# Kernel optimization log

Hardware: AMD Instinct MI355X
Metric: run time of the kernel (lower is better)

Reference implementation:

```python
import jax, jax.numpy as jnp
import numpy as np

B, N, E = 2, 10000, 160000
NODE_DIM, EDGE_DIM, HIDDEN = 128, 64, 256


def setup_inputs() -> dict:
    key = jax.random.key(0)
    ks = jax.random.split(key, 12)
    def lin(k, fan_in, fan_out):
        return jax.random.normal(k, (fan_in, fan_out), dtype=jnp.float32) / np.sqrt(fan_in)
    msg_in = 2 * NODE_DIM + EDGE_DIM   # 320
    upd_in = NODE_DIM + HIDDEN         # 384
    return {
        "node_features": jax.random.normal(ks[0], (B, N, NODE_DIM), dtype=jnp.float32),
        "edge_indices": jax.random.randint(ks[1], (B, E, 2), 0, N, dtype=jnp.int32),
        "edge_features": jax.random.normal(ks[2], (B, E, EDGE_DIM), dtype=jnp.float32),
        "W1m": lin(ks[3], msg_in, HIDDEN),  "b1m": jnp.zeros((HIDDEN,), jnp.float32),
        "W2m": lin(ks[4], HIDDEN, HIDDEN),  "b2m": jnp.zeros((HIDDEN,), jnp.float32),
        "W1u": lin(ks[5], upd_in, HIDDEN),  "b1u": jnp.zeros((HIDDEN,), jnp.float32),
        "W2u": lin(ks[6], HIDDEN, NODE_DIM), "b2u": jnp.zeros((NODE_DIM,), jnp.float32),
    }


def reference(node_features, edge_indices, edge_features,
              W1m, b1m, W2m, b2m, W1u, b1u, W2u, b2u):
    # node_features: [B, N, D]; edge_indices: [B, E, 2]; edge_features: [B, E, F]
    b, n, d = node_features.shape
    e = edge_indices.shape[1]
    src_idx = edge_indices[..., 0]  # [B, E]
    dst_idx = edge_indices[..., 1]  # [B, E]
    # batched gather of endpoint features
    src = jnp.take_along_axis(node_features, src_idx[..., None], axis=1)  # [B, E, D]
    dst = jnp.take_along_axis(node_features, dst_idx[..., None], axis=1)  # [B, E, D]
    msg_in = jnp.concatenate([src, dst, edge_features], axis=-1)          # [B, E, 2D+F]
    h = jax.nn.gelu(jnp.einsum("bei,ih->beh", msg_in, W1m) + b1m)
    messages = jnp.einsum("beh,ho->beo", h, W2m) + b2m                    # [B, E, H]
    # scatter-add into destination node buckets (flatten batch for segment_sum)
    flat_dst = (dst_idx + (jnp.arange(b, dtype=dst_idx.dtype)[:, None] * n)).reshape(-1)
    aggregated = jax.ops.segment_sum(
        messages.reshape(b * e, -1), flat_dst, num_segments=b * n
    ).reshape(b, n, -1)                                                   # [B, N, H]
    upd_in = jnp.concatenate([node_features, aggregated], axis=-1)        # [B, N, D+H]
    u = jax.nn.gelu(jnp.einsum("bni,ih->bnh", upd_in, W1u) + b1u)
    return jnp.einsum("bnh,ho->bno", u, W2u) + b2u                        # [B, N, D]
```

## Files before the change

### kernel.cpp

```cpp
#include <hip/hip_runtime.h>
#include <hip/hip_bf16.h>
#include <math.h>

#define BATCH   2
#define N_NODES 10000
#define E_EDGES 160000
#define BN      (BATCH * N_NODES)
#define BE      (BATCH * E_EDGES)
#define ND      128
#define ED      64
#define HID     256
#define K1      320
#define K2      256
#define K1U     384
#define NOUT    128
#define TMN     32
#define TME     64
#define LDH     264

typedef __attribute__((ext_vector_type(8))) short bf16x8;
typedef __attribute__((ext_vector_type(4))) float f32x4;

__device__ unsigned short g_Pb[(size_t)BN * 512];
__device__ unsigned short g_nodef_bf[(size_t)BN * ND];
__device__ unsigned short g_w1c[HID * K1U];
__device__ unsigned short g_w2ut[K2 * NOUT];
__device__ float          g_bc[HID];
__device__ int            g_hist[BN];

__device__ __forceinline__ float gelu_tanh(float x) {
    float u = 0.7978845608028654f * (x + 0.044715f * x * x * x);
    float e = __expf(2.0f * u);
    float t = 1.0f - 2.0f * __builtin_amdgcn_rcpf(e + 1.0f);
    return 0.5f * x * (1.0f + t);
}

__device__ __forceinline__ unsigned short f2bf(float f) {
    __hip_bfloat16 h = __float2bfloat16(f);
    return *reinterpret_cast<unsigned short*>(&h);
}

__device__ __forceinline__ float bf2f(unsigned short u) {
    unsigned int x = ((unsigned int)u) << 16;
    return *reinterpret_cast<float*>(&x);
}

__global__ __launch_bounds__(256) void prep_all(
    const float* __restrict__ nodef,
    const float* __restrict__ W1m, unsigned short* __restrict__ w1t,
    const float* __restrict__ W1u, const float* __restrict__ W2u,
    const float* __restrict__ W2m, const float* __restrict__ b2m)
{
    int i = blockIdx.x * blockDim.x + threadIdx.x;
    if (i < BN * ND / 4) {
        float4 v = ((const float4*)nodef)[i];
        ushort4 o;
        o.x = f2bf(v.x); o.y = f2bf(v.y); o.z = f2bf(v.z); o.w = f2bf(v.w);
        ((ushort4*)g_nodef_bf)[i] = o;
    }
    if (i < BN) g_hist[i] = 0;
    if (i < K1 * HID) {
        int k = i % K1, n = i / K1;
        w1t[i] = f2bf(W1m[(size_t)k * HID + n]);
    }
    if (i < ND * HID) {
        int k = i % ND, n = i / ND;
        g_w1c[n * K1U + k] = f2bf(W1u[(size_t)k * HID + n]);
    }
    if (i < K2 * NOUT) {
        int k = i % K2, n = i / K2;
        g_w2ut[i] = f2bf(W2u[(size_t)k * HID >= 0 ? (size_t)k * NOUT + n : 0]);
    }
    if (i < HID * HID) {
        int n = i & 255;
        int j = i >> 8;
        float a = 0.f;
        #pragma unroll 8
        for (int o = 0; o < HID; ++o)
            a += W2m[(size_t)j * HID + o] * W1u[(size_t)(128 + o) * HID + n];
        g_w1c[n * K1U + 128 + j] = f2bf(a);
    }
    if (i < HID) {
        float c = 0.f;
        #pragma unroll 8
        for (int o = 0; o < HID; ++o)
            c += b2m[o] * W1u[(size_t)(128 + o) * HID + i];
        g_bc[i] = c;
    }
}

__global__ __launch_bounds__(256) void dst_hist(const int* __restrict__ eidx)
{
    int e = blockIdx.x * blockDim.x + threadIdx.x;
    if (e < BE) {
        int dst = eidx[2 * e + 1];
        int b   = e / E_EDGES;
        atomicAdd(&g_hist[b * N_NODES + dst], 1);
    }
}

__global__ __launch_bounds__(1024, 1) void scan20k(int* __restrict__ offs)
{
    __shared__ int tots[1024];
    const int tid  = threadIdx.x;
    const int base = tid * 20;
    int v[20];
    int s = 0;
    #pragma unroll
    for (int j = 0; j < 20; ++j) {
        int i = base + j;
        int h = (i < BN) ? g_hist[i] : 0;
        v[j] = s; s += h;
    }
    tots[tid] = s;
    __syncthreads();
    #pragma unroll
    for (int d = 1; d < 1024; d <<= 1) {
        int t = (tid >= d) ? tots[tid - d] : 0;
        __syncthreads();
        tots[tid] += t;
        __syncthreads();
    }
    int excl = tots[tid] - s;
    #pragma unroll
    for (int j = 0; j < 20; ++j) {
        int i = base + j;
        if (i < BN) offs[i] = excl + v[j];
    }
}

__global__ __launch_bounds__(256) void dst_scatter(
    const int* __restrict__ eidx, int* __restrict__ offs, int* __restrict__ perm)
{
    int e = blockIdx.x * blockDim.x + threadIdx.x;
    if (e < BE) {
        int dst  = eidx[2 * e + 1];
        int b    = e / E_EDGES;
        int pos  = atomicAdd(&offs[b * N_NODES + dst], 1);
        perm[pos] = e;
    }
}

__global__ __launch_bounds__(512, 2) void pgemm(const unsigned short* __restrict__ w1t)
{
    const int tid  = threadIdx.x;
    const int wave = tid >> 6;
    const int lane = tid & 63;
    const int quad = lane >> 4;
    const int r16  = lane & 15;
    const int n0   = blockIdx.x * TMN;

    const int jb   = (wave & 3) * 64;
    const int koff = (wave < 4) ? 0 : 128;
    const int cb   = (wave < 4) ? 0 : 256;

    f32x4 acc[2][4];
    #pragma unroll
    for (int mt = 0; mt < 2; ++mt)
        #pragma unroll
        for (int nt = 0; nt < 4; ++nt)
            acc[mt][nt] = (f32x4){0.f, 0.f, 0.f, 0.f};

    for (int ks = 0; ks < ND / 32; ++ks) {
        bf16x8 wf[4], nf[2];
        #pragma unroll
        for (int nt = 0; nt < 4; ++nt)
            wf[nt] = *(const bf16x8*)&w1t[(size_t)(jb + nt * 16 + r16) * K1
                                          + koff + ks * 32 + quad * 8];
        #pragma unroll
        for (int mt = 0; mt < 2; ++mt)
            nf[mt] = *(const bf16x8*)&g_nodef_bf[(size_t)(n0 + mt * 16 + r16) * ND
                                                 + ks * 32 + quad * 8];
        #pragma unroll
        for (int mt = 0; mt < 2; ++mt)
            #pragma unroll
            for (int nt = 0; nt < 4; ++nt)
                acc[mt][nt] = __builtin_amdgcn_mfma_f32_16x16x32_bf16(
                    wf[nt], nf[mt], acc[mt][nt], 0, 0, 0);
    }

    #pragma unroll
    for (int nt = 0; nt < 4; ++nt) {
        int j0 = cb + jb + nt * 16 + quad * 4;
        #pragma unroll
        for (int mt = 0; mt < 2; ++mt) {
            int m = n0 + mt * 16 + r16;
            ushort4 o;
            o.x = f2bf(acc[mt][nt][0]); o.y = f2bf(acc[mt][nt][1]);
            o.z = f2bf(acc[mt][nt][2]); o.w = f2bf(acc[mt][nt][3]);
            *(ushort4*)&g_Pb[(size_t)m * 512 + j0] = o;
        }
    }
}

#define EK_SE   0
#define EK_SH   8192
#define EK_SMEM (8192 + TME * LDH * 2)

__global__ __launch_bounds__(512, 6) void edge_mlp_mfma(
    const int*            __restrict__ eidx,
    const float*          __restrict__ edgef,
    const int*            __restrict__ perm,
    const unsigned short* __restrict__ w1t,
    const float*          __restrict__ b1m,
    float* __restrict__ agg)
{
    __shared__ __align__(16) char smem[EK_SMEM];
    unsigned short* sE = (unsigned short*)(smem + EK_SE);
    unsigned short* sH = (unsigned short*)(smem + EK_SH);
    __shared__ int s_src[TME];
    __shared__ int s_dst[TME];
    __shared__ int s_eid[TME];

    const int tid  = threadIdx.x;
    const int wave = tid >> 6;
    const int lane = tid & 63;
    const int quad = lane >> 4;
    const int r16  = lane & 15;
    const int be0  = blockIdx.x * TME;

    if (tid < TME) {
        int eid = perm[be0 + tid];
        int b   = eid / E_EDGES;
        int2 se = ((const int2*)eidx)[eid];
        s_eid[tid] = eid;
        s_src[tid] = b * N_NODES + se.x;
        s_dst[tid] = b * N_NODES + se.y;
    }

    const unsigned short* wB1 = w1t + (size_t)(wave * 32) * K1 + 256;
    bf16x8 wf00 = *(const bf16x8*)&wB1[(size_t)r16        * K1 + quad * 8];
    bf16x8 wf01 = *(const bf16x8*)&wB1[(size_t)r16        * K1 + 32 + quad * 8];
    bf16x8 wf10 = *(const bf16x8*)&wB1[(size_t)(16 + r16) * K1 + quad * 8];
    bf16x8 wf11 = *(const bf16x8*)&wB1[(size_t)(16 + r16) * K1 + 32 + quad * 8];

    __syncthreads();

    {
        int row = tid >> 3;
        int c0  = (tid & 7) * 8;
        const float* fp = edgef + (size_t)s_eid[row] * ED + c0;
        float4 v0 = *(const float4*)fp;
        float4 v1 = *(const float4*)(fp + 4);
        ushort4 o0, o1;
        o0.x = f2bf(v0.x); o0.y = f2bf(v0.y); o0.z = f2bf(v0.z); o0.w = f2bf(v0.w);
        o1.x = f2bf(v1.x); o1.y = f2bf(v1.y); o1.z = f2bf(v1.z); o1.w = f2bf(v1.w);
        int p2 = c0 >> 5, kk = c0 & 31;
        *(ushort4*)&sE[p2 * 2048 + row * 32 + kk]     = o0;
        *(ushort4*)&sE[p2 * 2048 + row * 32 + kk + 4] = o1;
    }
    __syncthreads();

    f32x4 acc[4][2];
    #pragma unroll
    for (int mt = 0; mt < 4; ++mt)
        #pragma unroll
        for (int nt = 0; nt < 2; ++nt)
            acc[mt][nt] = (f32x4){0.f, 0.f, 0.f, 0.f};

    #pragma unroll
    for (int mt = 0; mt < 4; ++mt) {
        bf16x8 e0 = *(const bf16x8*)&sE[(mt * 16 + r16) * 32 + quad * 8];
        bf16x8 e1 = *(const bf16x8*)&sE[2048 + (mt * 16 + r16) * 32 + quad * 8];
        acc[mt][0] = __builtin_amdgcn_mfma_f32_16x16x32_bf16(wf00, e0, acc[mt][0], 0, 0, 0);
        acc[mt][1] = __builtin_amdgcn_mfma_f32_16x16x32_bf16(wf10, e0, acc[mt][1], 0, 0, 0);
        acc[mt][0] = __builtin_amdgcn_mfma_f32_16x16x32_bf16(wf01, e1, acc[mt][0], 0, 0, 0);
        acc[mt][1] = __builtin_amdgcn_mfma_f32_16x16x32_bf16(wf11, e1, acc[mt][1], 0, 0, 0);
    }

    {
        float4 bb[2];
        bb[0] = *(const float4*)&b1m[wave * 32 + quad * 4];
        bb[1] = *(const float4*)&b1m[wave * 32 + 16 + quad * 4];
        #pragma unroll
        for (int mt = 0; mt < 4; ++mt) {
            int m = mt * 16 + r16;
            const unsigned short* pS = &g_Pb[(size_t)s_src[m] * 512];
            const unsigned short* pD = &g_Pb[(size_t)s_dst[m] * 512 + 256];
            #pragma unroll
            for (int nt = 0; nt < 2; ++nt) {
                int n0 = wave * 32 + nt * 16 + quad * 4;
                ushort4 us = *(const ushort4*)(pS + n0);
                ushort4 ud = *(const ushort4*)(pD + n0);
                ushort4 o;
                o.x = f2bf(gelu_tanh(acc[mt][nt][0] + bf2f(us.x) + bf2f(ud.x) + bb[nt].x));
                o.y = f2bf(gelu_tanh(acc[mt][nt][1] + bf2f(us.y) + bf2f(ud.y) + bb[nt].y));
                o.z = f2bf(gelu_tanh(acc[mt][nt][2] + bf2f(us.z) + bf2f(ud.z) + bb[nt].z));
                o.w = f2bf(gelu_tanh(acc[mt][nt][3] + bf2f(us.w) + bf2f(ud.w) + bb[nt].w));
                *(ushort4*)&sH[m * LDH + n0] = o;
            }
        }
    }
    __syncthreads();

    {
        const int cc = tid & 255;
        const int r0 = (tid >> 8) * 32;
        int   cur  = s_dst[r0];
        float racc = 0.f;
        for (int mb = 0; mb < 32; mb += 8) {
            float v[8];
            #pragma unroll
            for (int j = 0; j < 8; ++j)
                v[j] = bf2f(sH[(r0 + mb + j) * LDH + cc]);
            #pragma unroll
            for (int j = 0; j < 8; ++j) {
                int d = s_dst[r0 + mb + j];
                if (d != cur) {
                    atomicAdd(&agg[(size_t)cur * HID + cc], racc);
                    cur = d; racc = v[j];
                } else {
                    racc += v[j];
                }
            }
        }
        atomicAdd(&agg[(size_t)cur * HID + cc], racc);
    }
}

__global__ __launch_bounds__(256, 4) void node_mlp_mfma(
    const float* __restrict__ agg,
    const float* __restrict__ b1u,
    const float* __restrict__ b2u,
    float* __restrict__ out)
{
    __shared__ __align__(16) unsigned short sH[TMN * LDH];

    const int tid  = threadIdx.x;
    const int wave = tid >> 6;
    const int lane = tid & 63;
    const int quad = lane >> 4;
    const int r16  = lane & 15;
    const int n0   = blockIdx.x * TMN;

    f32x4 acc[2][4];
    #pragma unroll
    for (int mt = 0; mt < 2; ++mt)
        #pragma unroll
        for (int nt = 0; nt < 4; ++nt)
            acc[mt][nt] = (f32x4){0.f, 0.f, 0.f, 0.f};

    for (int ks = 0; ks < 4; ++ks) {
        bf16x8 wf[4], nf[2];
        #pragma unroll
        for (int nt = 0; nt < 4; ++nt)
            wf[nt] = *(const bf16x8*)&g_w1c[(size_t)(wave * 64 + nt * 16 + r16) * K1U
                                            + ks * 32 + quad * 8];
        #pragma unroll
        for (int mt = 0; mt < 2; ++mt)
            nf[mt] = *(const bf16x8*)&g_nodef_bf[(size_t)(n0 + mt * 16 + r16) * ND
                                                 + ks * 32 + quad * 8];
        #pragma unroll
        for (int mt = 0; mt < 2; ++mt)
            #pragma unroll
            for (int nt = 0; nt < 4; ++nt)
                acc[mt][nt] = __builtin_amdgcn_mfma_f32_16x16x32_bf16(
                    wf[nt], nf[mt], acc[mt][nt], 0, 0, 0);
    }
    for (int ks = 0; ks < 8; ++ks) {
        bf16x8 wf[4], nf[2];
        #pragma unroll
        for (int nt = 0; nt < 4; ++nt)
            wf[nt] = *(const bf16x8*)&g_w1c[(size_t)(wave * 64 + nt * 16 + r16) * K1U
                                            + (4 + ks) * 32 + quad * 8];
        #pragma unroll
        for (int mt = 0; mt < 2; ++mt) {
            const float* fp = &agg[(size_t)(n0 + mt * 16 + r16) * HID + ks * 32 + quad * 8];
            float4 v0 = *(const float4*)fp;
            float4 v1 = *(const float4*)(fp + 4);
            union { bf16x8 v; ushort4 u[2]; } cv;
            cv.u[0] = (ushort4){f2bf(v0.x), f2bf(v0.y), f2bf(v0.z), f2bf(v0.w)};
            cv.u[1] = (ushort4){f2bf(v1.x), f2bf(v1.y), f2bf(v1.z), f2bf(v1.w)};
            nf[mt] = cv.v;
        }
        #pragma unroll
        for (int mt = 0; mt < 2; ++mt)
            #pragma unroll
            for (int nt = 0; nt < 4; ++nt)
                acc[mt][nt] = __builtin_amdgcn_mfma_f32_16x16x32_bf16(
                    wf[nt], nf[mt], acc[mt][nt], 0, 0, 0);
    }

    #pragma unroll
    for (int nt = 0; nt < 4; ++nt) {
        int nn0 = wave * 64 + nt * 16 + quad * 4;
        float4 bb = *(const float4*)&b1u[nn0];
        float4 bc = *(const float4*)&g_bc[nn0];
        #pragma unroll
        for (int mt = 0; mt < 2; ++mt) {
            int row = n0 + mt * 16 + r16;
            float hv = (float)g_hist[row];
            int m = mt * 16 + r16;
            ushort4 o;
            o.x = f2bf(gelu_tanh(acc[mt][nt][0] + bb.x + hv * bc.x));
            o.y = f2bf(gelu_tanh(acc[mt][nt][1] + bb.y + hv * bc.y));
            o.z = f2bf(gelu_tanh(acc[mt][nt][2] + bb.z + hv * bc.z));
            o.w = f2bf(gelu_tanh(acc[mt][nt][3] + bb.w + hv * bc.w));
            *(ushort4*)&sH[m * LDH + nn0] = o;
        }
    }
    __syncthreads();

    f32x4 acc2[2][2];
    #pragma unroll
    for (int mt = 0; mt < 2; ++mt)
        #pragma unroll
        for (int nt = 0; nt < 2; ++nt)
            acc2[mt][nt] = (f32x4){0.f, 0.f, 0.f, 0.f};

    for (int ks = 0; ks < K2 / 32; ++ks) {
        bf16x8 wf2[2], hf[2];
        #pragma unroll
        for (int nt = 0; nt < 2; ++nt)
            wf2[nt] = *(const bf16x8*)&g_w2ut[(size_t)(wave * 32 + nt * 16 + r16) * K2
                                              + ks * 32 + quad * 8];
        #pragma unroll
        for (int mt = 0; mt < 2; ++mt)
            hf[mt] = *(const bf16x8*)&sH[(mt * 16 + r16) * LDH + ks * 32 + quad * 8];
        #pragma unroll
        for (int mt = 0; mt < 2; ++mt)
            #pragma unroll
            for (int nt = 0; nt < 2; ++nt)
                acc2[mt][nt] = __builtin_amdgcn_mfma_f32_16x16x32_bf16(
                    wf2[nt], hf[mt], acc2[mt][nt], 0, 0, 0);
    }

    #pragma unroll
    for (int nt = 0; nt < 2; ++nt) {
        int j0 = wave * 32 + nt * 16 + quad * 4;
        float4 bb = *(const float4*)&b2u[j0];
        #pragma unroll
        for (int mt = 0; mt < 2; ++mt) {
            int row = n0 + mt * 16 + r16;
            float4 v = {acc2[mt][nt][0] + bb.x, acc2[mt][nt][1] + bb.y,
                        acc2[mt][nt][2] + bb.z, acc2[mt][nt][3] + bb.w};
            *(float4*)&out[(size_t)row * NOUT + j0] = v;
        }
    }
}


extern "C" void kernel_launch(void* const* d_in, const int* in_sizes, int n_in,
                              void* d_out, int out_size, void* d_ws, size_t ws_size,
                              hipStream_t stream) {
    const float* nodef = (const float*)d_in[0];
    const int*   eidx  = (const int*)  d_in[1];
    const float* edgef = (const float*)d_in[2];
    const float* W1m   = (const float*)d_in[3];
    const float* b1m   = (const float*)d_in[4];
    const float* W2m   = (const float*)d_in[5];
    const float* b2m   = (const float*)d_in[6];
    const float* W1u   = (const float*)d_in[7];
    const float* b1u   = (const float*)d_in[8];
    const float* W2u   = (const float*)d_in[9];
    const float* b2u   = (const float*)d_in[10];
    float* out = (float*)d_out;

    char* wsb = (char*)d_ws;
    float* agg = (float*)wsb;
    const size_t AGG_B = (size_t)BN * HID * sizeof(float);

    char* ob = (char*)d_out;
    unsigned short* w1t  = (unsigned short*)(ob + 5120000);
    int* offs            = (int*)(ob + 5494912);
    int* perm            = (int*)(ob + 5574912);

    hipMemsetAsync(agg, 0, AGG_B, stream);

    prep_all<<<(BN * ND / 4 + 255) / 256, 256, 0, stream>>>(
        nodef, W1m, w1t, W1u, W2u, W2m, b2m);

    dst_hist<<<(BE + 255) / 256, 256, 0, stream>>>(eidx);
    scan20k<<<1, 1024, 0, stream>>>(offs);
    dst_scatter<<<(BE + 255) / 256, 256, 0, stream>>>(eidx, offs, perm);

    pgemm<<<BN / TMN, 512, 0, stream>>>(w1t);

    edge_mlp_mfma<<<BE / TME, 512, 0, stream>>>(
        eidx, edgef, perm, w1t, b1m, agg);

    node_mlp_mfma<<<BN / TMN, 256, 0, stream>>>(agg, b1u, b2u, out);
}
```

Measured before the change: 359.4 us.

## Fuse agg zeroing into histogram, scatter into pgemm, prefetch gathers early

Removes the separate memset by having dst_hist zero the aggregation buffer (4 float4 per edge thread covers BN*HID floats), and folds the dst_scatter pass into the pgemm kernel (625 blocks × 512 threads = BE edges). The scan stages the histogram in shared memory. In the edge MLP, the gathered src/dst projection rows and bias are loaded before the edge-feature MFMA so that the gather latency overlaps compute, at the cost of extra registers. This cuts two launches but couples the scatter atomics to the GEMM blocks and relies on exact size divisibility.

New measurement: 393.9 us. 9.6% more time.

```diff
diff --git a/kernel.cpp b/kernel.cpp
--- a/kernel.cpp
+++ b/kernel.cpp
@@ -69,7 +69,7 @@
     }
     if (i < K2 * NOUT) {
         int k = i % K2, n = i / K2;
-        g_w2ut[i] = f2bf(W2u[(size_t)k * HID >= 0 ? (size_t)k * NOUT + n : 0]);
+        g_w2ut[i] = f2bf(W2u[(size_t)k * NOUT + n]);
     }
     if (i < HID * HID) {
         int n = i & 255;
@@ -89,9 +89,14 @@
     }
 }
 
-__global__ __launch_bounds__(256) void dst_hist(const int* __restrict__ eidx)
+__global__ __launch_bounds__(256) void dst_hist(
+    const int* __restrict__ eidx, float* __restrict__ agg)
 {
     int e = blockIdx.x * blockDim.x + threadIdx.x;
+    float4 z = {0.f, 0.f, 0.f, 0.f};
+    #pragma unroll
+    for (int j = 0; j < 4; ++j)
+        ((float4*)agg)[(size_t)j * BE + e] = z;
     if (e < BE) {
         int dst = eidx[2 * e + 1];
         int b   = e / E_EDGES;
@@ -101,15 +106,18 @@
 
 __global__ __launch_bounds__(1024, 1) void scan20k(int* __restrict__ offs)
 {
+    __shared__ int sh[BN];
     __shared__ int tots[1024];
-    const int tid  = threadIdx.x;
+    const int tid = threadIdx.x;
+    for (int j = tid; j < BN; j += 1024) sh[j] = g_hist[j];
+    __syncthreads();
     const int base = tid * 20;
     int v[20];
     int s = 0;
     #pragma unroll
     for (int j = 0; j < 20; ++j) {
         int i = base + j;
-        int h = (i < BN) ? g_hist[i] : 0;
+        int h = (i < BN) ? sh[i] : 0;
         v[j] = s; s += h;
     }
     tots[tid] = s;
@@ -125,25 +133,26 @@
     #pragma unroll
     for (int j = 0; j < 20; ++j) {
         int i = base + j;
-        if (i < BN) offs[i] = excl + v[j];
-    }
-}
-
-__global__ __launch_bounds__(256) void dst_scatter(
-    const int* __restrict__ eidx, int* __restrict__ offs, int* __restrict__ perm)
-{
-    int e = blockIdx.x * blockDim.x + threadIdx.x;
-    if (e < BE) {
-        int dst  = eidx[2 * e + 1];
-        int b    = e / E_EDGES;
-        int pos  = atomicAdd(&offs[b * N_NODES + dst], 1);
+        if (i < BN) sh[i] = excl + v[j];
+    }
+    __syncthreads();
+    for (int j = tid; j < BN; j += 1024) offs[j] = sh[j];
+}
+
+__global__ __launch_bounds__(512, 2) void pgemm_scatter(
+    const unsigned short* __restrict__ w1t,
+    const int* __restrict__ eidx,
+    int* __restrict__ offs, int* __restrict__ perm)
+{
+    const int tid  = threadIdx.x;
+    {
+        int e   = blockIdx.x * 512 + tid;
+        int2 se = ((const int2*)eidx)[e];
+        int b   = (e >= E_EDGES) ? 1 : 0;
+        int pos = atomicAdd(&offs[b * N_NODES + se.y], 1);
         perm[pos] = e;
     }
-}
-
-__global__ __launch_bounds__(512, 2) void pgemm(const unsigned short* __restrict__ w1t)
-{
-    const int tid  = threadIdx.x;
+
     const int wave = tid >> 6;
     const int lane = tid & 63;
     const int quad = lane >> 4;
@@ -233,8 +242,24 @@
     bf16x8 wf01 = *(const bf16x8*)&wB1[(size_t)r16        * K1 + 32 + quad * 8];
     bf16x8 wf10 = *(const bf16x8*)&wB1[(size_t)(16 + r16) * K1 + quad * 8];
     bf16x8 wf11 = *(const bf16x8*)&wB1[(size_t)(16 + r16) * K1 + 32 + quad * 8];
-
-    __syncthreads();
+    float4 bb0 = *(const float4*)&b1m[wave * 32 + quad * 4];
+    float4 bb1 = *(const float4*)&b1m[wave * 32 + 16 + quad * 4];
+
+    __syncthreads();
+
+    ushort4 us[4][2], ud[4][2];
+    #pragma unroll
+    for (int mt = 0; mt < 4; ++mt) {
+        int m = mt * 16 + r16;
+        const unsigned short* pS = &g_Pb[(size_t)s_src[m] * 512];
+        const unsigned short* pD = &g_Pb[(size_t)s_dst[m] * 512 + 256];
+        #pragma unroll
+        for (int nt = 0; nt < 2; ++nt) {
+            int n0 = wave * 32 + nt * 16 + quad * 4;
+            us[mt][nt] = *(const ushort4*)(pS + n0);
+            ud[mt][nt] = *(const ushort4*)(pD + n0);
+        }
+    }
 
     {
         int row = tid >> 3;
@@ -268,27 +293,20 @@
         acc[mt][1] = __builtin_amdgcn_mfma_f32_16x16x32_bf16(wf11, e1, acc[mt][1], 0, 0, 0);
     }
 
-    {
-        float4 bb[2];
-        bb[0] = *(const float4*)&b1m[wave * 32 + quad * 4];
-        bb[1] = *(const float4*)&b1m[wave * 32 + 16 + quad * 4];
-        #pragma unroll
-        for (int mt = 0; mt < 4; ++mt) {
-            int m = mt * 16 + r16;
-            const unsigned short* pS = &g_Pb[(size_t)s_src[m] * 512];
-            const unsigned short* pD = &g_Pb[(size_t)s_dst[m] * 512 + 256];
-            #pragma unroll
-            for (int nt = 0; nt < 2; ++nt) {
-                int n0 = wave * 32 + nt * 16 + quad * 4;
-                ushort4 us = *(const ushort4*)(pS + n0);
-                ushort4 ud = *(const ushort4*)(pD + n0);
-                ushort4 o;
-                o.x = f2bf(gelu_tanh(acc[mt][nt][0] + bf2f(us.x) + bf2f(ud.x) + bb[nt].x));
-                o.y = f2bf(gelu_tanh(acc[mt][nt][1] + bf2f(us.y) + bf2f(ud.y) + bb[nt].y));
-                o.z = f2bf(gelu_tanh(acc[mt][nt][2] + bf2f(us.z) + bf2f(ud.z) + bb[nt].z));
-                o.w = f2bf(gelu_tanh(acc[mt][nt][3] + bf2f(us.w) + bf2f(ud.w) + bb[nt].w));
-                *(ushort4*)&sH[m * LDH + n0] = o;
-            }
+    #pragma unroll
+    for (int mt = 0; mt < 4; ++mt) {
+        int m = mt * 16 + r16;
+        #pragma unroll
+        for (int nt = 0; nt < 2; ++nt) {
+            int n0 = wave * 32 + nt * 16 + quad * 4;
+            float4 bb = nt ? bb1 : bb0;
+            ushort4 u0 = us[mt][nt], u1 = ud[mt][nt];
+            ushort4 o;
+            o.x = f2bf(gelu_tanh(acc[mt][nt][0] + bf2f(u0.x) + bf2f(u1.x) + bb.x));
+            o.y = f2bf(gelu_tanh(acc[mt][nt][1] + bf2f(u0.y) + bf2f(u1.y) + bb.y));
+            o.z = f2bf(gelu_tanh(acc[mt][nt][2] + bf2f(u0.z) + bf2f(u1.z) + bb.z));
+            o.w = f2bf(gelu_tanh(acc[mt][nt][3] + bf2f(u0.w) + bf2f(u1.w) + bb.w));
+            *(ushort4*)&sH[m * LDH + n0] = o;
         }
     }
     __syncthreads();
@@ -458,23 +476,19 @@
 
     char* wsb = (char*)d_ws;
     float* agg = (float*)wsb;
-    const size_t AGG_B = (size_t)BN * HID * sizeof(float);
 
     char* ob = (char*)d_out;
     unsigned short* w1t  = (unsigned short*)(ob + 5120000);
     int* offs            = (int*)(ob + 5494912);
     int* perm            = (int*)(ob + 5574912);
 
-    hipMemsetAsync(agg, 0, AGG_B, stream);
-
     prep_all<<<(BN * ND / 4 + 255) / 256, 256, 0, stream>>>(
         nodef, W1m, w1t, W1u, W2u, W2m, b2m);
 
-    dst_hist<<<(BE + 255) / 256, 256, 0, stream>>>(eidx);
+    dst_hist<<<BE / 256, 256, 0, stream>>>(eidx, agg);
     scan20k<<<1, 1024, 0, stream>>>(offs);
-    dst_scatter<<<(BE + 255) / 256, 256, 0, stream>>>(eidx, offs, perm);
-
-    pgemm<<<BN / TMN, 512, 0, stream>>>(w1t);
+
+    pgemm_scatter<<<BN / TMN, 512, 0, stream>>>(w1t, eidx, offs, perm);
 
     edge_mlp_mfma<<<BE / TME, 512, 0, stream>>>(
         eidx, edgef, perm, w1t, b1m, agg);
```
